# Optimization experiments

Measured on AMD Instinct MI355X. Metric: run time of the kernel, lower is better.

Reference implementation:

```python
import jax, jax.numpy as jnp
import numpy as np

EPS = 1e-12

def _l2norm(v, axis):
    return v / jnp.maximum(jnp.linalg.norm(v, axis=axis, keepdims=True), EPS)

def setup_inputs() -> dict:
    key = jax.random.key(0)
    k1, k2, k3 = jax.random.split(key, 3)
    B, D, C = 65536, 768, 100
    P = C * (C - 1) // 2  # 4950 pairwise local heads
    x = jax.random.normal(k1, (B, D), dtype=jnp.float32)
    first_out = jax.random.normal(k2, (B, C), dtype=jnp.float32)
    weights = jax.random.normal(k3, (P, 2, D), dtype=jnp.float32) * (1.0 / np.sqrt(D))
    sigma = jnp.ones((P,), dtype=jnp.float32)
    return {"x": x, "first_out": first_out, "weights": weights, "sigma": sigma, "cur_stage": 4}

def reference(x, first_out, weights, sigma, cur_stage):
    # top-2 class indices per sample, sorted ascending -> pair key (a, b), a < b
    _, top2 = jax.lax.top_k(first_out, 2)              # [B, 2]
    sorted_idx = jnp.sort(top2, axis=1)                # [B, 2]
    a = sorted_idx[:, 0]
    b = sorted_idx[:, 1]
    pair_idx = b * (b - 1) // 2 + a                    # key 'a-b' -> flat head index
    W = weights[pair_idx]                              # [B, 2, D] gathered expert weights
    s = sigma[pair_idx]                                # [B]
    # CosineLinear (use_RP=False): sigma * normalize(x) @ normalize(W)^T
    xn = _l2norm(x, axis=1)                            # [B, D]
    Wn = _l2norm(W, axis=2)                            # [B, 2, D]
    logits = s[:, None] * jnp.einsum('bd,bkd->bk', xn, Wn)  # [B, 2]
    # pick which of the two candidate classes the local head prefers
    sel = jnp.argmax(logits, axis=1)                   # [B]
    preds = jnp.take_along_axis(sorted_idx, sel[:, None], axis=1)[:, 0]  # [B]
    return preds, logits
```

## Files before the change

### kernel.cpp

```cpp
#include <hip/hip_runtime.h>
#include <math.h>


#define D_DIM 768
#define C_DIM 100
#define P_DIM 4950
#define F4_PER_ROW (D_DIM / 4)
#define EPS_N 1e-12

__device__ __forceinline__ bool vi_gt(float v0, int i0, float v1, int i1) {
    return (v0 > v1) || (v0 == v1 && i0 < i1);
}

__global__ __launch_bounds__(256) void norm_kernel(
    const float* __restrict__ weights,
    double* __restrict__ invn,
    int nrows)
{
    const int lane = threadIdx.x & 63;
    const int row = (blockIdx.x << 2) + (threadIdx.x >> 6);
    if (row >= nrows) return;

    const float4* wv = (const float4*)(weights + (size_t)row * D_DIM);
    double n = 0.0;
    #pragma unroll
    for (int j = 0; j < 3; ++j) {
        float4 w = wv[lane + j * 64];
        n += (double)w.x * w.x + (double)w.y * w.y
           + (double)w.z * w.z + (double)w.w * w.w;
    }
    #pragma unroll
    for (int m = 1; m < 64; m <<= 1) n += __shfl_xor(n, m, 64);
    if (lane == 0) invn[row] = 1.0 / fmax(sqrt(n), EPS_N);
}

__global__ __launch_bounds__(256) void top2_kernel(
    const float* __restrict__ first_out,
    int* __restrict__ abbuf,
    int B)
{
    const int lane = threadIdx.x & 63;
    const int r = (blockIdx.x << 2) + (threadIdx.x >> 6);
    if (r >= B) return;

    const float* fo = first_out + (size_t)r * C_DIM;
    float e0 = fo[lane];
    int   j1 = lane + 64;
    float e1 = (j1 < C_DIM) ? fo[j1] : -INFINITY;

    float v1, v2; int i1, i2;
    if (vi_gt(e1, j1, e0, lane)) { v1 = e1; i1 = j1;   v2 = e0; i2 = lane; }
    else                         { v1 = e0; i1 = lane; v2 = e1; i2 = j1; }

    #pragma unroll
    for (int m = 1; m < 64; m <<= 1) {
        float ov1 = __shfl_xor(v1, m, 64);
        int   oi1 = __shfl_xor(i1, m, 64);
        float ov2 = __shfl_xor(v2, m, 64);
        int   oi2 = __shfl_xor(i2, m, 64);
        if (vi_gt(ov1, oi1, v1, i1)) {
            float nv2; int ni2;
            if (vi_gt(v1, i1, ov2, oi2)) { nv2 = v1;  ni2 = i1; }
            else                         { nv2 = ov2; ni2 = oi2; }
            v1 = ov1; i1 = oi1; v2 = nv2; i2 = ni2;
        } else {
            if (vi_gt(ov1, oi1, v2, i2)) { v2 = ov1; i2 = oi1; }
        }
    }
    if (lane == 0) {
        const int a = min(i1, i2);
        const int b = max(i1, i2);
        abbuf[r] = a | (b << 16);
    }
}

__global__ __launch_bounds__(256) void main_kernel(
    const float* __restrict__ x,
    const float* __restrict__ weights,
    const float* __restrict__ sigma,
    const double* __restrict__ invn,
    const int* __restrict__ abbuf,
    float* __restrict__ out,
    int B)
{
    const int lane = threadIdx.x & 63;
    const int r = (blockIdx.x << 2) + (threadIdx.x >> 6);
    if (r >= B) return;

    const int ab = abbuf[r];
    const int a = ab & 0xffff;
    const int b = ab >> 16;
    const int pair = b * (b - 1) / 2 + a;

    const float4* xv = (const float4*)(x + (size_t)r * D_DIM);
    const float4* w0 = (const float4*)(weights + (size_t)pair * (2 * D_DIM));
    const float4* w1 = w0 + F4_PER_ROW;

    float  xx = 0.0f;
    double d0 = 0.0, d1 = 0.0;
    #pragma unroll
    for (int j = 0; j < 3; ++j) {
        const int idx = lane + j * 64;
        float4 xa = xv[idx];
        float4 wa = w0[idx];
        float4 wb = w1[idx];
        xx += xa.x * xa.x + xa.y * xa.y + xa.z * xa.z + xa.w * xa.w;
        d0 += (double)xa.x * wa.x + (double)xa.y * wa.y
            + (double)xa.z * wa.z + (double)xa.w * wa.w;
        d1 += (double)xa.x * wb.x + (double)xa.y * wb.y
            + (double)xa.z * wb.z + (double)xa.w * wb.w;
    }
    #pragma unroll
    for (int m = 1; m < 64; m <<= 1) {
        xx += __shfl_xor(xx, m, 64);
        d0 += __shfl_xor(d0, m, 64);
        d1 += __shfl_xor(d1, m, 64);
    }

    if (lane == 0) {
        double s    = (double)sigma[pair];
        double sinx = s / fmax(sqrt((double)xx), EPS_N);
        double l0   = sinx * d0 * invn[2 * pair];
        double l1   = sinx * d1 * invn[2 * pair + 1];
        int sel = (l1 > l0) ? 1 : 0;
        out[r] = (float)(sel ? b : a);
        out[B + 2 * r]     = (float)l0;
        out[B + 2 * r + 1] = (float)l1;
    }
}

extern "C" void kernel_launch(void* const* d_in, const int* in_sizes, int n_in,
                              void* d_out, int out_size, void* d_ws, size_t ws_size,
                              hipStream_t stream) {
    const float* x         = (const float*)d_in[0];
    const float* first_out = (const float*)d_in[1];
    const float* weights   = (const float*)d_in[2];
    const float* sigma     = (const float*)d_in[3];
    float* out = (float*)d_out;

    const int B = in_sizes[0] / D_DIM;
    const int NW = 2 * P_DIM;

    double* invn = (double*)d_ws;
    int* abbuf   = (int*)((char*)d_ws + (size_t)NW * sizeof(double));

    hipLaunchKernelGGL(norm_kernel, dim3((NW + 3) / 4), dim3(256), 0, stream,
                       weights, invn, NW);
    hipLaunchKernelGGL(top2_kernel, dim3((B + 3) / 4), dim3(256), 0, stream,
                       first_out, abbuf, B);
    hipLaunchKernelGGL(main_kernel, dim3((B + 3) / 4), dim3(256), 0, stream,
                       x, weights, sigma, invn, abbuf, out, B);
}
```

Baseline: 335.7 us.

## Process two rows per wave in top2 and main kernels, use nontemporal x loads

New measurement: 353.5 us. 1.05x slower.

```diff
diff --git a/kernel.cpp b/kernel.cpp
--- a/kernel.cpp
+++ b/kernel.cpp
@@ -7,6 +7,8 @@
 #define P_DIM 4950
 #define F4_PER_ROW (D_DIM / 4)
 #define EPS_N 1e-12
+
+typedef float vf4 __attribute__((ext_vector_type(4)));
 
 __device__ __forceinline__ bool vi_gt(float v0, int i0, float v1, int i1) {
     return (v0 > v1) || (v0 == v1 && i0 < i1);
@@ -21,11 +23,11 @@
     const int row = (blockIdx.x << 2) + (threadIdx.x >> 6);
     if (row >= nrows) return;
 
-    const float4* wv = (const float4*)(weights + (size_t)row * D_DIM);
+    const vf4* wv = (const vf4*)(weights + (size_t)row * D_DIM);
     double n = 0.0;
     #pragma unroll
     for (int j = 0; j < 3; ++j) {
-        float4 w = wv[lane + j * 64];
+        vf4 w = wv[lane + j * 64];
         n += (double)w.x * w.x + (double)w.y * w.y
            + (double)w.z * w.z + (double)w.w * w.w;
     }
@@ -40,24 +42,37 @@
     int B)
 {
     const int lane = threadIdx.x & 63;
-    const int r = (blockIdx.x << 2) + (threadIdx.x >> 6);
+    const int wave = threadIdx.x >> 6;
+    const int l32 = lane & 31;
+    const int r = (((blockIdx.x << 2) + wave) << 1) + (lane >> 5);
     if (r >= B) return;
 
     const float* fo = first_out + (size_t)r * C_DIM;
-    float e0 = fo[lane];
-    int   j1 = lane + 64;
-    float e1 = (j1 < C_DIM) ? fo[j1] : -INFINITY;
 
-    float v1, v2; int i1, i2;
-    if (vi_gt(e1, j1, e0, lane)) { v1 = e1; i1 = j1;   v2 = e0; i2 = lane; }
-    else                         { v1 = e0; i1 = lane; v2 = e1; i2 = j1; }
+    float v1 = fo[l32]; int i1 = l32;
+    float v2 = -INFINITY; int i2 = 0x7fffffff;
+    {
+        float e = fo[l32 + 32]; int ie = l32 + 32;
+        if (vi_gt(e, ie, v1, i1)) { v2 = v1; i2 = i1; v1 = e; i1 = ie; }
+        else if (vi_gt(e, ie, v2, i2)) { v2 = e; i2 = ie; }
+    }
+    {
+        float e = fo[l32 + 64]; int ie = l32 + 64;
+        if (vi_gt(e, ie, v1, i1)) { v2 = v1; i2 = i1; v1 = e; i1 = ie; }
+        else if (vi_gt(e, ie, v2, i2)) { v2 = e; i2 = ie; }
+    }
+    if (l32 < 4) {
+        float e = fo[l32 + 96]; int ie = l32 + 96;
+        if (vi_gt(e, ie, v1, i1)) { v2 = v1; i2 = i1; v1 = e; i1 = ie; }
+        else if (vi_gt(e, ie, v2, i2)) { v2 = e; i2 = ie; }
+    }
 
     #pragma unroll
-    for (int m = 1; m < 64; m <<= 1) {
-        float ov1 = __shfl_xor(v1, m, 64);
-        int   oi1 = __shfl_xor(i1, m, 64);
-        float ov2 = __shfl_xor(v2, m, 64);
-        int   oi2 = __shfl_xor(i2, m, 64);
+    for (int m = 1; m < 32; m <<= 1) {
+        float ov1 = __shfl_xor(v1, m, 32);
+        int   oi1 = __shfl_xor(i1, m, 32);
+        float ov2 = __shfl_xor(v2, m, 32);
+        int   oi2 = __shfl_xor(i2, m, 32);
         if (vi_gt(ov1, oi1, v1, i1)) {
             float nv2; int ni2;
             if (vi_gt(v1, i1, ov2, oi2)) { nv2 = v1;  ni2 = i1; }
@@ -67,7 +82,7 @@
             if (vi_gt(ov1, oi1, v2, i2)) { v2 = ov1; i2 = oi1; }
         }
     }
-    if (lane == 0) {
+    if (l32 == 0) {
         const int a = min(i1, i2);
         const int b = max(i1, i2);
         abbuf[r] = a | (b << 16);
@@ -84,48 +99,69 @@
     int B)
 {
     const int lane = threadIdx.x & 63;
-    const int r = (blockIdx.x << 2) + (threadIdx.x >> 6);
-    if (r >= B) return;
+    const int wave = threadIdx.x >> 6;
+    const int base = ((blockIdx.x << 2) + wave) << 1;
+    if (base >= B) return;
 
-    const int ab = abbuf[r];
-    const int a = ab & 0xffff;
-    const int b = ab >> 16;
-    const int pair = b * (b - 1) / 2 + a;
+    const int ab0 = abbuf[base];
+    const int ab1 = abbuf[base + 1];
+    const int a0 = ab0 & 0xffff, b0 = ab0 >> 16;
+    const int a1 = ab1 & 0xffff, b1 = ab1 >> 16;
+    const int p0 = b0 * (b0 - 1) / 2 + a0;
+    const int p1 = b1 * (b1 - 1) / 2 + a1;
 
-    const float4* xv = (const float4*)(x + (size_t)r * D_DIM);
-    const float4* w0 = (const float4*)(weights + (size_t)pair * (2 * D_DIM));
-    const float4* w1 = w0 + F4_PER_ROW;
+    const vf4* xv  = (const vf4*)(x + (size_t)base * D_DIM);
+    const vf4* w0v = (const vf4*)(weights + (size_t)p0 * (2 * D_DIM));
+    const vf4* w1v = (const vf4*)(weights + (size_t)p1 * (2 * D_DIM));
 
-    float  xx = 0.0f;
-    double d0 = 0.0, d1 = 0.0;
+    float  xx0 = 0.f, xx1 = 0.f;
+    double d00 = 0.0, d01 = 0.0, d10 = 0.0, d11 = 0.0;
     #pragma unroll
     for (int j = 0; j < 3; ++j) {
         const int idx = lane + j * 64;
-        float4 xa = xv[idx];
-        float4 wa = w0[idx];
-        float4 wb = w1[idx];
-        xx += xa.x * xa.x + xa.y * xa.y + xa.z * xa.z + xa.w * xa.w;
-        d0 += (double)xa.x * wa.x + (double)xa.y * wa.y
-            + (double)xa.z * wa.z + (double)xa.w * wa.w;
-        d1 += (double)xa.x * wb.x + (double)xa.y * wb.y
-            + (double)xa.z * wb.z + (double)xa.w * wb.w;
+        vf4 xa = __builtin_nontemporal_load(xv + idx);
+        vf4 xb = __builtin_nontemporal_load(xv + F4_PER_ROW + idx);
+        vf4 wa = w0v[idx];
+        vf4 wb = w0v[F4_PER_ROW + idx];
+        vf4 wc = w1v[idx];
+        vf4 wd = w1v[F4_PER_ROW + idx];
+        xx0 += xa.x * xa.x + xa.y * xa.y + xa.z * xa.z + xa.w * xa.w;
+        xx1 += xb.x * xb.x + xb.y * xb.y + xb.z * xb.z + xb.w * xb.w;
+        d00 += (double)xa.x * wa.x + (double)xa.y * wa.y
+             + (double)xa.z * wa.z + (double)xa.w * wa.w;
+        d01 += (double)xa.x * wb.x + (double)xa.y * wb.y
+             + (double)xa.z * wb.z + (double)xa.w * wb.w;
+        d10 += (double)xb.x * wc.x + (double)xb.y * wc.y
+             + (double)xb.z * wc.z + (double)xb.w * wc.w;
+        d11 += (double)xb.x * wd.x + (double)xb.y * wd.y
+             + (double)xb.z * wd.z + (double)xb.w * wd.w;
     }
     #pragma unroll
     for (int m = 1; m < 64; m <<= 1) {
-        xx += __shfl_xor(xx, m, 64);
-        d0 += __shfl_xor(d0, m, 64);
-        d1 += __shfl_xor(d1, m, 64);
+        xx0 += __shfl_xor(xx0, m, 64);
+        xx1 += __shfl_xor(xx1, m, 64);
+        d00 += __shfl_xor(d00, m, 64);
+        d01 += __shfl_xor(d01, m, 64);
+        d10 += __shfl_xor(d10, m, 64);
+        d11 += __shfl_xor(d11, m, 64);
     }
 
-    if (lane == 0) {
-        double s    = (double)sigma[pair];
-        double sinx = s / fmax(sqrt((double)xx), EPS_N);
-        double l0   = sinx * d0 * invn[2 * pair];
-        double l1   = sinx * d1 * invn[2 * pair + 1];
-        int sel = (l1 > l0) ? 1 : 0;
-        out[r] = (float)(sel ? b : a);
-        out[B + 2 * r]     = (float)l0;
-        out[B + 2 * r + 1] = (float)l1;
+    if (lane < 2) {
+        const int    rr  = base + lane;
+        const int    p   = lane ? p1 : p0;
+        const int    aa  = lane ? a1 : a0;
+        const int    bb  = lane ? b1 : b0;
+        const float  xxv = lane ? xx1 : xx0;
+        const double dd0 = lane ? d10 : d00;
+        const double dd1 = lane ? d11 : d01;
+        const double s    = (double)sigma[p];
+        const double sinx = s / fmax(sqrt((double)xxv), EPS_N);
+        const double l0   = sinx * dd0 * invn[2 * p];
+        const double l1   = sinx * dd1 * invn[2 * p + 1];
+        const int sel = (l1 > l0) ? 1 : 0;
+        out[rr] = (float)(sel ? bb : aa);
+        out[B + 2 * rr]     = (float)l0;
+        out[B + 2 * rr + 1] = (float)l1;
     }
 }
 
@@ -138,7 +174,7 @@
     const float* sigma     = (const float*)d_in[3];
     float* out = (float*)d_out;
 
-    const int B = in_sizes[0] / D_DIM;
+    const int B  = in_sizes[0] / D_DIM;
     const int NW = 2 * P_DIM;
 
     double* invn = (double*)d_ws;
@@ -146,8 +182,8 @@
 
     hipLaunchKernelGGL(norm_kernel, dim3((NW + 3) / 4), dim3(256), 0, stream,
                        weights, invn, NW);
-    hipLaunchKernelGGL(top2_kernel, dim3((B + 3) / 4), dim3(256), 0, stream,
+    hipLaunchKernelGGL(top2_kernel, dim3((B + 7) / 8), dim3(256), 0, stream,
                        first_out, abbuf, B);
-    hipLaunchKernelGGL(main_kernel, dim3((B + 3) / 4), dim3(256), 0, stream,
+    hipLaunchKernelGGL(main_kernel, dim3((B + 7) / 8), dim3(256), 0, stream,
                        x, weights, sigma, invn, abbuf, out, B);
 }
```
